# Performance work log

Measured on AMD Instinct MI355X. Metric: run time of the kernel, lower is better.

The kernel has to match this reference:

```python
import jax, jax.numpy as jnp
import numpy as np

QMAX = 127.0


def setup_inputs() -> dict:
    key = jax.random.key(0)
    k1, k2, k3, k4, k5, k6 = jax.random.split(key, 6)
    B, IN, OUT = 8192, 4096, 4096
    # Quantized activation (uint8-range values stored as float, per-sample asymmetric quant)
    x_q = jax.random.randint(k1, (B, IN), 0, 256).astype(jnp.float32)
    x_scale = jax.random.uniform(k2, (B,), dtype=jnp.float32, minval=0.001, maxval=0.02)
    x_zp = jax.random.randint(k3, (B,), 0, 256).astype(jnp.float32)
    # Symmetric per-tensor int8 weight (values in [-127, 127]) + scalar scale
    w_q = jax.random.randint(k4, (OUT, IN), -127, 128).astype(jnp.float32)
    w_scale = jax.random.uniform(k5, (1,), dtype=jnp.float32, minval=0.001, maxval=0.02)
    fp_bias = jax.random.normal(k6, (OUT,), dtype=jnp.float32)
    return {"x_q": x_q, "x_scale": x_scale, "x_zp": x_zp, "w_q": w_q,
            "w_scale": w_scale, "fp_bias": fp_bias}


def reference(x_q, x_scale, x_zp, w_q, w_scale, fp_bias):
    # zero-point subtraction (per-sample)
    xt = x_q - x_zp[:, None]                      # [B, IN]
    # integer GEMM (values are integers held in float32)
    lin = xt @ w_q.T                              # [B, OUT]
    # integer bias: round(fp_bias / (w_scale * x_scale))
    qbias = jnp.round(fp_bias[None, :] / (w_scale[0] * x_scale[:, None]))  # [B, OUT]
    lin = lin + qbias
    # requantize: symmetric per-tensor int8
    s = jnp.max(jnp.abs(lin)) / QMAX
    q = jnp.clip(jnp.round(lin / s), -QMAX, QMAX)  # [B, OUT]
    out_scale = s * x_scale * w_scale[0]           # [B]
    zero_point = jnp.zeros_like(out_scale)
    return q, out_scale, zero_point
```

## Files before the change

kernel.cpp:

```cpp
#include <hip/hip_runtime.h>
#include <hip/hip_bf16.h>


typedef int i32x4 __attribute__((ext_vector_type(4)));

#define AS1 __attribute__((address_space(1)))
#define AS3 __attribute__((address_space(3)))

__device__ __forceinline__ void async16(const void* g, void* lds) {
    __builtin_amdgcn_global_load_lds((const AS1 void*)g, (AS3 void*)lds, 16, 0, 0);
}

__global__ void conv_x_kernel(const float4* __restrict__ xq, int* __restrict__ x8,
                              int* gmax, int n4) {
    int i = blockIdx.x * 256 + threadIdx.x;
    if (i == 0) *gmax = 0;
    if (i >= n4) return;
    float4 v = xq[i];
    int b0 = ((int)v.x - 128) & 255;
    int b1 = ((int)v.y - 128) & 255;
    int b2 = ((int)v.z - 128) & 255;
    int b3 = ((int)v.w - 128) & 255;
    x8[i] = b0 | (b1 << 8) | (b2 << 16) | (b3 << 24);
}

__global__ void conv_w_kernel(const float* __restrict__ wq, int* __restrict__ w8,
                              int* __restrict__ rowsum, int K) {
    int row = blockIdx.x;
    int t = threadIdx.x;
    const float4* src = (const float4*)(wq + (size_t)row * K);
    int* dst = w8 + (size_t)row * (K >> 2);
    int sum = 0;
    int passes = K >> 10;
    for (int p = 0; p < passes; ++p) {
        float4 v = src[p * 256 + t];
        int b0 = (int)v.x, b1 = (int)v.y, b2 = (int)v.z, b3 = (int)v.w;
        sum += b0 + b1 + b2 + b3;
        dst[p * 256 + t] = (b0 & 255) | ((b1 & 255) << 8) | ((b2 & 255) << 16) | ((b3 & 255) << 24);
    }
    #pragma unroll
    for (int m = 32; m; m >>= 1) sum += __shfl_xor(sum, m, 64);
    __shared__ int wsum[4];
    if ((t & 63) == 0) wsum[t >> 6] = sum;
    __syncthreads();
    if (t == 0) rowsum[row] = wsum[0] + wsum[1] + wsum[2] + wsum[3];
}

__global__ __launch_bounds__(512, 2) void gemm_i8_kernel(
    const char* __restrict__ x8, const char* __restrict__ w8,
    const int* __restrict__ w_rowsum,
    const float* __restrict__ x_scale, const float* __restrict__ x_zp,
    const float* __restrict__ fp_bias, const float* __restrict__ w_scale_p,
    int* __restrict__ lin_out, int* gmax, int N, int K) {
    __shared__ __align__(16) char lds[4][32768];
    __shared__ int s_bmax;

    const int t = threadIdx.x;
    const int w = t >> 6, l = t & 63;
    if (t == 0) s_bmax = 0;

    const int nwg = gridDim.x;
    const int bid = blockIdx.x;
    int swz = bid;
    if ((nwg & 7) == 0) { const int cpx = nwg >> 3; swz = (bid & 7) * cpx + (bid >> 3); }
    const int ntn = N >> 8;
    const int tm = swz / ntn, tn = swz % ntn;

    const int nt = K >> 6;

    const int srow = (w << 5) + (l >> 2);
    const int phys = (l & 3) ^ ((l >> 3) & 3);
    const char* pA0 = x8 + (size_t)(tm * 256 + srow) * K + phys * 16;
    const char* pA1 = pA0 + (size_t)16 * K;
    const char* pB0 = w8 + (size_t)(tn * 256 + srow) * K + phys * 16;
    const char* pB1 = pB0 + (size_t)16 * K;
    const int dA0 = (w << 11) + (l << 4);
    const int dA1 = dA0 + 1024;

    const int lane_lo = l & 15, lane_hi = l >> 4;
    const int wm = w >> 2, wn = w & 3;
    const int sl = (lane_hi ^ ((lane_lo >> 1) & 3)) << 4;
    const int abase = (wm * 128 + lane_lo) * 64 + sl;
    const int bbase = 16384 + (wn * 64 + lane_lo) * 64 + sl;

    i32x4 acc[8][4] = {};

    #pragma unroll
    for (int g = 0; g < 3; ++g) {
        char* buf = lds[g];
        const size_t koff = (size_t)g * 64;
        async16(pA0 + koff, buf + dA0);
        async16(pA1 + koff, buf + dA1);
        async16(pB0 + koff, buf + 16384 + dA0);
        async16(pB1 + koff, buf + 16384 + dA1);
    }

    for (int j = 0; j < nt; ++j) {
        asm volatile("s_waitcnt lgkmcnt(0)" ::: "memory");
        if (j + 2 < nt)       asm volatile("s_waitcnt vmcnt(8)" ::: "memory");
        else if (j + 2 == nt) asm volatile("s_waitcnt vmcnt(4)" ::: "memory");
        else                  asm volatile("s_waitcnt vmcnt(0)" ::: "memory");
        __builtin_amdgcn_s_barrier();
        asm volatile("" ::: "memory");
        if (j + 3 < nt) {
            char* buf = lds[(j + 3) & 3];
            const size_t koff = (size_t)(j + 3) * 64;
            async16(pA0 + koff, buf + dA0);
            async16(pA1 + koff, buf + dA1);
            async16(pB0 + koff, buf + 16384 + dA0);
            async16(pB1 + koff, buf + 16384 + dA1);
        }
        const char* buf = lds[j & 3];
        i32x4 af[8], bf[4];
        #pragma unroll
        for (int m = 0; m < 8; ++m) af[m] = *(const i32x4*)(buf + abase + m * 1024);
        #pragma unroll
        for (int n = 0; n < 4; ++n) bf[n] = *(const i32x4*)(buf + bbase + n * 1024);
        __builtin_amdgcn_s_setprio(1);
        #pragma unroll
        for (int m = 0; m < 8; ++m)
            #pragma unroll
            for (int n = 0; n < 4; ++n)
                acc[m][n] = __builtin_amdgcn_mfma_i32_16x16x64_i8(af[m], bf[n], acc[m][n], 0, 0, 0);
        __builtin_amdgcn_s_setprio(0);
    }

    const float ws = *w_scale_p;
    const int rowg0 = tm * 256 + wm * 128 + lane_hi * 4;
    const int colg0 = tn * 256 + wn * 64 + lane_lo;
    float fb[4]; int wrs[4];
    #pragma unroll
    for (int n = 0; n < 4; ++n) {
        fb[n] = fp_bias[colg0 + n * 16];
        wrs[n] = w_rowsum[colg0 + n * 16];
    }
    int lmax = 0;
    #pragma unroll
    for (int m = 0; m < 8; ++m) {
        #pragma unroll
        for (int r = 0; r < 4; ++r) {
            const int row = rowg0 + m * 16 + r;
            const float xs = x_scale[row];
            const int zz = 128 - (int)x_zp[row];
            const float d = ws * xs;
            int* orow = lin_out + (size_t)row * N + colg0;
            #pragma unroll
            for (int n = 0; n < 4; ++n) {
                const int qb = (int)rintf(fb[n] / d);
                const int lin = acc[m][n][r] + zz * wrs[n] + qb;
                const int a = lin < 0 ? -lin : lin;
                lmax = a > lmax ? a : lmax;
                orow[n * 16] = lin;
            }
        }
    }
    atomicMax(&s_bmax, lmax);
    __syncthreads();
    if (t == 0) atomicMax(gmax, s_bmax);
}

__global__ void requant_kernel(float4* qout, const int4* lin, const int* gmax, int n4) {
    int i = blockIdx.x * 256 + threadIdx.x;
    if (i >= n4) return;
    float s = (float)(*gmax) / 127.0f;
    int4 v = lin[i];
    float4 o;
    o.x = fminf(127.0f, fmaxf(-127.0f, rintf((float)v.x / s)));
    o.y = fminf(127.0f, fmaxf(-127.0f, rintf((float)v.y / s)));
    o.z = fminf(127.0f, fmaxf(-127.0f, rintf((float)v.z / s)));
    o.w = fminf(127.0f, fmaxf(-127.0f, rintf((float)v.w / s)));
    qout[i] = o;
}

__global__ void scale_kernel(float* __restrict__ out_scale, float* __restrict__ out_zp,
                             const float* __restrict__ x_scale,
                             const float* __restrict__ w_scale_p,
                             const int* gmax, int B) {
    int i = blockIdx.x * 256 + threadIdx.x;
    if (i >= B) return;
    float s = (float)(*gmax) / 127.0f;
    out_scale[i] = s * x_scale[i] * w_scale_p[0];
    out_zp[i] = 0.0f;
}

extern "C" void kernel_launch(void* const* d_in, const int* in_sizes, int n_in,
                              void* d_out, int out_size, void* d_ws, size_t ws_size,
                              hipStream_t stream) {
    const float* x_q     = (const float*)d_in[0];
    const float* x_scale = (const float*)d_in[1];
    const float* x_zp    = (const float*)d_in[2];
    const float* w_q     = (const float*)d_in[3];
    const float* w_scale = (const float*)d_in[4];
    const float* fp_bias = (const float*)d_in[5];

    const int B   = in_sizes[1];
    const int IN  = in_sizes[0] / B;
    const int OUT = in_sizes[5];

    float* q         = (float*)d_out;
    float* out_scale = q + (size_t)B * OUT;
    float* out_zp    = out_scale + B;

    char* ws    = (char*)d_ws;
    int* gmax   = (int*)ws;
    char* x8    = ws + 64;
    char* w8    = x8 + (size_t)B * IN;
    int* rowsum = (int*)(w8 + (size_t)OUT * IN);
    size_t needed = 64 + (size_t)B * IN + (size_t)OUT * IN + (size_t)OUT * 4;
    if (ws_size < needed) return;

    int n4x = (B * IN) >> 2;
    conv_x_kernel<<<(n4x + 255) / 256, 256, 0, stream>>>((const float4*)x_q, (int*)x8, gmax, n4x);
    conv_w_kernel<<<OUT, 256, 0, stream>>>(w_q, (int*)w8, rowsum, IN);

    int nblocks = (B / 256) * (OUT / 256);
    gemm_i8_kernel<<<nblocks, 512, 0, stream>>>(x8, w8, rowsum, x_scale, x_zp, fp_bias,
                                                w_scale, (int*)q, gmax, OUT, IN);

    int n4q = (B * OUT) >> 2;
    requant_kernel<<<(n4q + 255) / 256, 256, 0, stream>>>((float4*)q, (const int4*)q, gmax, n4q);
    scale_kernel<<<(B + 255) / 256, 256, 0, stream>>>(out_scale, out_zp, x_scale, w_scale, gmax, B);
}
```

Baseline: 273.8 us.

## Switch GEMM main loop to BK=128 double buffer with phased interleaving

The int8 GEMM mainloop changes from a 4-stage ring of 64-wide K tiles to a 2-stage double buffer of 128-wide K tiles. It uses a new XOR swizzle and splits each iteration into four phases. In each phase the async global-to-LDS loads for the next tile are interleaved with LDS fragment reads and MFMA bursts, separated by barriers and sched_barriers, so memory and compute overlap more finely and each barrier covers more work. The cost is a shallower prefetch depth and more barriers per iteration. LDS use stays at 128KB, so occupancy is unchanged.

```diff
diff --git a/kernel.cpp b/kernel.cpp
--- a/kernel.cpp
+++ b/kernel.cpp
@@ -52,7 +52,7 @@
     const float* __restrict__ x_scale, const float* __restrict__ x_zp,
     const float* __restrict__ fp_bias, const float* __restrict__ w_scale_p,
     int* __restrict__ lin_out, int* gmax, int N, int K) {
-    __shared__ __align__(16) char lds[4][32768];
+    __shared__ __align__(16) char lds[2][65536];
     __shared__ int s_bmax;
 
     const int t = threadIdx.x;
@@ -66,63 +66,78 @@
     const int ntn = N >> 8;
     const int tm = swz / ntn, tn = swz % ntn;
 
-    const int nt = K >> 6;
-
-    const int srow = (w << 5) + (l >> 2);
-    const int phys = (l & 3) ^ ((l >> 3) & 3);
-    const char* pA0 = x8 + (size_t)(tm * 256 + srow) * K + phys * 16;
-    const char* pA1 = pA0 + (size_t)16 * K;
-    const char* pB0 = w8 + (size_t)(tn * 256 + srow) * K + phys * 16;
-    const char* pB1 = pB0 + (size_t)16 * K;
-    const int dA0 = (w << 11) + (l << 4);
-    const int dA1 = dA0 + 1024;
+    const int nt = K >> 7;
+
+    const int row_t = t >> 3;
+    const int g_t = (t & 7) ^ (row_t & 7);
+    const char* gA = x8 + (size_t)(tm * 256 + row_t) * K + g_t * 16;
+    const char* gB = w8 + (size_t)(tn * 256 + row_t) * K + g_t * 16;
+    const int dst_t = t * 16;
 
     const int lane_lo = l & 15, lane_hi = l >> 4;
     const int wm = w >> 2, wn = w & 3;
-    const int sl = (lane_hi ^ ((lane_lo >> 1) & 3)) << 4;
-    const int abase = (wm * 128 + lane_lo) * 64 + sl;
-    const int bbase = 16384 + (wn * 64 + lane_lo) * 64 + sl;
+    const int swz0 = ((lane_hi) ^ (lane_lo & 7)) << 4;
+    const int swz1 = ((4 + lane_hi) ^ (lane_lo & 7)) << 4;
+    const int abase = (wm * 128 + lane_lo) * 128;
+    const int bbase = 32768 + (wn * 64 + lane_lo) * 128;
 
     i32x4 acc[8][4] = {};
 
     #pragma unroll
-    for (int g = 0; g < 3; ++g) {
-        char* buf = lds[g];
-        const size_t koff = (size_t)g * 64;
-        async16(pA0 + koff, buf + dA0);
-        async16(pA1 + koff, buf + dA1);
-        async16(pB0 + koff, buf + 16384 + dA0);
-        async16(pB1 + koff, buf + 16384 + dA1);
-    }
+    for (int i = 0; i < 4; ++i) {
+        async16(gA + (size_t)(i * 64) * K, lds[0] + i * 8192 + dst_t);
+        async16(gB + (size_t)(i * 64) * K, lds[0] + 32768 + i * 8192 + dst_t);
+    }
+    asm volatile("s_waitcnt vmcnt(0)" ::: "memory");
+    __builtin_amdgcn_s_barrier();
 
     for (int j = 0; j < nt; ++j) {
-        asm volatile("s_waitcnt lgkmcnt(0)" ::: "memory");
-        if (j + 2 < nt)       asm volatile("s_waitcnt vmcnt(8)" ::: "memory");
-        else if (j + 2 == nt) asm volatile("s_waitcnt vmcnt(4)" ::: "memory");
-        else                  asm volatile("s_waitcnt vmcnt(0)" ::: "memory");
-        __builtin_amdgcn_s_barrier();
-        asm volatile("" ::: "memory");
-        if (j + 3 < nt) {
-            char* buf = lds[(j + 3) & 3];
-            const size_t koff = (size_t)(j + 3) * 64;
-            async16(pA0 + koff, buf + dA0);
-            async16(pA1 + koff, buf + dA1);
-            async16(pB0 + koff, buf + 16384 + dA0);
-            async16(pB1 + koff, buf + 16384 + dA1);
+        const char* buf = lds[j & 1];
+        char* nbuf = lds[(j + 1) & 1];
+        const size_t koff = (size_t)(j + 1) << 7;
+        const bool more = (j + 1) < nt;
+        i32x4 bf[4][2];
+
+        #pragma unroll
+        for (int p = 0; p < 4; ++p) {
+            if (p == 0) {
+                #pragma unroll
+                for (int n = 0; n < 4; ++n) {
+                    bf[n][0] = *(const i32x4*)(buf + bbase + n * 2048 + swz0);
+                    bf[n][1] = *(const i32x4*)(buf + bbase + n * 2048 + swz1);
+                }
+            }
+            i32x4 af0_0 = *(const i32x4*)(buf + abase + (2 * p) * 2048 + swz0);
+            i32x4 af0_1 = *(const i32x4*)(buf + abase + (2 * p) * 2048 + swz1);
+            i32x4 af1_0 = *(const i32x4*)(buf + abase + (2 * p + 1) * 2048 + swz0);
+            i32x4 af1_1 = *(const i32x4*)(buf + abase + (2 * p + 1) * 2048 + swz1);
+            if (p == 0 && more) {
+                #pragma unroll
+                for (int i = 0; i < 4; ++i)
+                    async16(gA + (size_t)(i * 64) * K + koff, nbuf + i * 8192 + dst_t);
+            }
+            if (p == 1 && more) {
+                #pragma unroll
+                for (int i = 0; i < 4; ++i)
+                    async16(gB + (size_t)(i * 64) * K + koff, nbuf + 32768 + i * 8192 + dst_t);
+            }
+            __builtin_amdgcn_s_barrier();
+            asm volatile("s_waitcnt lgkmcnt(0)" ::: "memory");
+            __builtin_amdgcn_sched_barrier(0);
+            __builtin_amdgcn_s_setprio(1);
+            #pragma unroll
+            for (int n = 0; n < 4; ++n) {
+                acc[2 * p][n]     = __builtin_amdgcn_mfma_i32_16x16x64_i8(af0_0, bf[n][0], acc[2 * p][n], 0, 0, 0);
+                acc[2 * p][n]     = __builtin_amdgcn_mfma_i32_16x16x64_i8(af0_1, bf[n][1], acc[2 * p][n], 0, 0, 0);
+                acc[2 * p + 1][n] = __builtin_amdgcn_mfma_i32_16x16x64_i8(af1_0, bf[n][0], acc[2 * p + 1][n], 0, 0, 0);
+                acc[2 * p + 1][n] = __builtin_amdgcn_mfma_i32_16x16x64_i8(af1_1, bf[n][1], acc[2 * p + 1][n], 0, 0, 0);
+            }
+            __builtin_amdgcn_s_setprio(0);
+            if (p == 3) {
+                asm volatile("s_waitcnt vmcnt(0)" ::: "memory");
+            }
+            __builtin_amdgcn_s_barrier();
         }
-        const char* buf = lds[j & 3];
-        i32x4 af[8], bf[4];
-        #pragma unroll
-        for (int m = 0; m < 8; ++m) af[m] = *(const i32x4*)(buf + abase + m * 1024);
-        #pragma unroll
-        for (int n = 0; n < 4; ++n) bf[n] = *(const i32x4*)(buf + bbase + n * 1024);
-        __builtin_amdgcn_s_setprio(1);
-        #pragma unroll
-        for (int m = 0; m < 8; ++m)
-            #pragma unroll
-            for (int n = 0; n < 4; ++n)
-                acc[m][n] = __builtin_amdgcn_mfma_i32_16x16x64_i8(af[m], bf[n], acc[m][n], 0, 0, 0);
-        __builtin_amdgcn_s_setprio(0);
     }
 
     const float ws = *w_scale_p;
```

Result: faster. 257.4 us (-6.0%).
